# Optimization experiments

Measured on AMD Instinct MI355X. Metric: run time of the kernel, lower is better.

## Reference

```python
import jax, jax.numpy as jnp
import numpy as np
from jax import lax

B, P, NB, NF, NC, R = 128, 2048, 2000, 250, 16, 128
LS = NB - NF  # number of simulated bins = len_bins_gensig - 1


def setup_inputs() -> dict:
    key = jax.random.key(0)
    ks = jax.random.split(key, 10)
    return {
        'batched_stim_spat': jax.random.normal(ks[0], (B, P), jnp.float32),
        'stim_time': jax.random.normal(ks[1], (NB,), jnp.float32),
        'batched_initial_spike_section': (jax.random.uniform(ks[2], (B, NF)) < 0.05).astype(jnp.float32),
        'batched_coupling_cells': (jax.random.uniform(ks[3], (B, NC, NB)) < 0.05).astype(jnp.float32),
        'spatial_filter': jax.random.normal(ks[4], (P,), jnp.float32) * 0.02,
        'spatial_bias': jnp.float32(-2.0),
        'stim_timecourse_filter': jax.random.normal(ks[5], (NF,), jnp.float32) * 0.1,
        'feedback_filter': jax.random.normal(ks[6], (NF,), jnp.float32) * 0.05 - 0.02,
        'coupling_filter': jax.random.normal(ks[7], (NC, NF), jnp.float32) * 0.05,
        'u': jax.random.uniform(ks[8], (LS, B, R), jnp.float32),
        'n_repeats': R,
    }


def _corr1d_valid(x, k):
    # torch F.conv1d is cross-correlation; lax conv is too (no kernel flip)
    # x: (n,), k: (m,) -> (n - m + 1,)
    out = lax.conv_general_dilated(x[None, None, :], k[None, None, :], (1,), 'VALID',
                                   dimension_numbers=('NCH', 'OIH', 'NCH'))
    return out[0, 0]


def reference(batched_stim_spat, stim_time, batched_initial_spike_section,
              batched_coupling_cells, spatial_filter, spatial_bias,
              stim_timecourse_filter, feedback_filter, coupling_filter, u, n_repeats):
    nf = stim_timecourse_filter.shape[0]

    # stimulus time component: (n_bins - nf + 1,)
    filt_time = _corr1d_valid(stim_time, stim_timecourse_filter)

    # spatial exp arg for separable linear-spatial GLM:
    # einsum('bpt,p->bt', stim_spat[:,:,None]*filt_time, spatial_filter)
    # factors into outer product of (stim_spat @ spatial_filter) and filt_time
    stim_gensig = (batched_stim_spat @ spatial_filter)[:, None] * filt_time[None, :] + spatial_bias  # (B, T)

    # coupling exp arg: conv1d over all coupled cells -> (B, T)
    coup = lax.conv_general_dilated(batched_coupling_cells, coupling_filter[None, :, :], (1,), 'VALID',
                                    dimension_numbers=('NCH', 'OIH', 'NCH'))[:, 0, :]

    gensig_piece = stim_gensig + coup  # (B, T) with T = n_bins - nf + 1
    len_sim = gensig_piece.shape[1] - 1

    # initial feedback window: last nf spike bins, broadcast over repeats
    batch = batched_stim_spat.shape[0]
    w0 = jnp.broadcast_to(batched_initial_spike_section[:, None, :], (batch, n_repeats, nf)) + 0.0

    def step(window, xs):
        g_t, u_t = xs  # (B,), (B, R)
        fb = jnp.einsum('brk,k->br', window, feedback_filter)
        g = g_t[:, None] + fb
        spike = (u_t < jax.nn.sigmoid(g)).astype(window.dtype)  # Bernoulli(sigmoid(g))
        window = jnp.concatenate([window[:, :, 1:], spike[:, :, None]], axis=2)
        return window, spike

    xs = (jnp.swapaxes(gensig_piece[:, :len_sim], 0, 1), u[:len_sim])  # ((LS,B), (LS,B,R))
    _, spikes = lax.scan(step, w0, xs)  # spikes: (LS, B, R)

    out = jnp.concatenate([w0, jnp.moveaxis(spikes, 0, 2)], axis=2)  # (B, R, n_bins)
    return out
```

## Files before the change

### kernel.cpp

```cpp
#include <hip/hip_runtime.h>
#include <math.h>

#define B_  128
#define P_  2048
#define NB_ 2000
#define NF_ 250
#define NC_ 16
#define R_  128
#define LS_ 1750
#define NT_ 1751
#define BR_ (B_ * R_)
#define H_  16

typedef int v4i __attribute__((ext_vector_type(4)));

template <int CTRL>
__device__ __forceinline__ long long dpp64i(long long x) {
    int lo = (int)x, hi = (int)(x >> 32);
    lo = __builtin_amdgcn_mov_dpp(lo, CTRL, 0xF, 0xF, true);
    hi = __builtin_amdgcn_mov_dpp(hi, CTRL, 0xF, 0xF, true);
    return ((long long)(unsigned)lo) | ((long long)hi << 32);
}

__device__ __forceinline__ double logit_fast(float uf) {
    double u = (double)uf;
    double v = 1.0 - u;
    double qd = u / v;
    long long bits = __double_as_longlong(qd);
    int e = (int)((bits >> 52) & 0x7FF) - 1023;
    double m = __longlong_as_double((bits & 0xFFFFFFFFFFFFFLL) | 0x3FF0000000000000LL);
    if (m > 1.4142135623730951) { m *= 0.5; e += 1; }
    double s = (m - 1.0) / (m + 1.0);
    double z = s * s;
    double Q = fma(z, fma(z, fma(z, fma(z, fma(z, fma(z,
        0.06666666666666667, 0.07692307692307693), 0.09090909090909091),
        0.1111111111111111), 0.14285714285714285), 0.2), 0.3333333333333333);
    double logm = fma(2.0 * s, z * Q, 2.0 * s);
    return fma((double)e, 0.6931471805599453, logm);
}

__device__ __forceinline__ long long thrq_of(double lu, double fb) {
    double thr = lu - fb;
    thr = fmin(fmax(thr, -8.0), 8.0);
    double d = fma(thr, 0x1p45, 0x1.8p52);
    return (__double_as_longlong(d) & 0xFFFFFFFFFFFFFLL) - (1LL << 51);
}

__global__ __launch_bounds__(256) void k_pre(const float* __restrict__ st,
                                             const float* __restrict__ stf,
                                             const float* __restrict__ sp,
                                             const float* __restrict__ sf,
                                             double* __restrict__ ft,
                                             double* __restrict__ sdot) {
    if (blockIdx.x < 7) {
        int t = blockIdx.x * 256 + threadIdx.x;
        if (t >= NT_) return;
        double s = 0.0;
        for (int k = 0; k < NF_; ++k) s += (double)st[t + k] * (double)stf[k];
        ft[t] = s;
    } else {
        __shared__ double red[256];
        int b = blockIdx.x - 7;
        double s = 0.0;
        for (int p = threadIdx.x; p < P_; p += 256)
            s += (double)sp[(size_t)b * P_ + p] * (double)sf[p];
        red[threadIdx.x] = s;
        __syncthreads();
        for (int off = 128; off > 0; off >>= 1) {
            if (threadIdx.x < off) red[threadIdx.x] += red[threadIdx.x + off];
            __syncthreads();
        }
        if (threadIdx.x == 0) sdot[b] = red[0];
    }
}

__global__ __launch_bounds__(256) void k_coup(const float* __restrict__ cc,
                                              const float* __restrict__ cf,
                                              const double* __restrict__ sdot,
                                              const double* __restrict__ ft,
                                              const float* __restrict__ bias,
                                              double* __restrict__ gensig) {
    __shared__ __align__(16) float  ccs[NC_ * 512];
    __shared__ __align__(16) double cfs[NC_ * 256];
    __shared__ double red[3][64][4];
    int b = blockIdx.y, t0 = blockIdx.x * 256;
    int tid = threadIdx.x, lane = tid & 63, wv = tid >> 6;

    for (int idx = tid; idx < NC_ * 128; idx += 256) {
        int c = idx >> 7, j4 = (idx & 127) * 4, src = t0 + j4;
        const float* p = cc + ((size_t)b * NC_ + c) * NB_ + src;
        float4 v;
        if (src + 3 < NB_) v = *(const float4*)p;
        else {
            v.x = (src     < NB_) ? p[0] : 0.f;
            v.y = (src + 1 < NB_) ? p[1] : 0.f;
            v.z = (src + 2 < NB_) ? p[2] : 0.f;
            v.w = (src + 3 < NB_) ? p[3] : 0.f;
        }
        *(float4*)&ccs[c * 512 + j4] = v;
    }
    for (int idx = tid; idx < NC_ * 256; idx += 256) {
        int c = idx >> 8, k = idx & 255;
        cfs[idx] = (k < NF_) ? (double)cf[c * NF_ + k] : 0.0;
    }
    __syncthreads();

    double a0 = 0, a1 = 0, a2 = 0, a3 = 0;
    int base = lane * 4;
    for (int c = wv; c < NC_; c += 4) {
        const float*  row  = &ccs[c * 512];
        const double* crow = &cfs[c * 256];
        float4 cur = *(const float4*)&row[base];
        for (int k4 = 0; k4 < 252; k4 += 4) {
            float4 nxt = *(const float4*)&row[base + k4 + 4];
            double e0 = cur.x, e1 = cur.y, e2 = cur.z, e3 = cur.w;
            double e4 = nxt.x, e5 = nxt.y, e6 = nxt.z;
            double c0 = crow[k4], c1 = crow[k4 + 1], c2 = crow[k4 + 2], c3 = crow[k4 + 3];
            a0 += e0 * c0 + e1 * c1 + e2 * c2 + e3 * c3;
            a1 += e1 * c0 + e2 * c1 + e3 * c2 + e4 * c3;
            a2 += e2 * c0 + e3 * c1 + e4 * c2 + e5 * c3;
            a3 += e3 * c0 + e4 * c1 + e5 * c2 + e6 * c3;
            cur = nxt;
        }
    }
    if (wv > 0) {
        red[wv - 1][lane][0] = a0; red[wv - 1][lane][1] = a1;
        red[wv - 1][lane][2] = a2; red[wv - 1][lane][3] = a3;
    }
    __syncthreads();
    if (wv == 0) {
        a0 += red[0][lane][0] + red[1][lane][0] + red[2][lane][0];
        a1 += red[0][lane][1] + red[1][lane][1] + red[2][lane][1];
        a2 += red[0][lane][2] + red[1][lane][2] + red[2][lane][2];
        a3 += red[0][lane][3] + red[1][lane][3] + red[2][lane][3];
        double gb = (double)bias[0];
        double sd = sdot[b];
        double accs[4] = {a0, a1, a2, a3};
        int tb = t0 + base;
        for (int i = 0; i < 4; ++i) {
            int t = tb + i;
            if (t < LS_) gensig[(size_t)b * LS_ + t] = sd * ft[t] + gb + accs[i];
        }
    }
}

__global__ __launch_bounds__(256, 1) void k_scan(const double* __restrict__ gensig,
                                                 const float* __restrict__ u,
                                                 const float* __restrict__ iss,
                                                 const float* __restrict__ ff,
                                                 float* __restrict__ out) {
    __shared__ double farT_all[4][16 * 17];
    int tid = threadIdx.x;
    int wv = tid >> 6, l = tid & 63;
    int gw = blockIdx.x * 4 + wv;
    int b = gw >> 3, rbase = (gw & 7) * 16;
    double* farT = &farT_all[wv][0];

    int lw = l & 15;
    int q  = l >> 4;
    int cn = l >> 2;
    int j  = l & 3;

    const float* issb = iss + b * NF_;
    for (int idx = l; idx < 16 * NF_; idx += 64) {
        int c = idx / NF_, k = idx - c * NF_;
        out[((size_t)(b * R_ + rbase + c)) * NB_ + k] = issb[k];
    }

    unsigned long long W0 = 0, W1 = 0, W2 = 0, W3 = 0;
    for (int k = 0; k < NF_; ++k) {
        unsigned long long bit = (issb[k] > 0.5f) ? 1ull : 0ull;
        if      (k <  64) W0 |= bit << k;
        else if (k < 128) W1 |= bit << (k - 64);
        else if (k < 192) W2 |= bit << (k - 128);
        else              W3 |= bit << (k - 192);
    }

    int Bword[4][6][4];
#pragma unroll
    for (int kc = 0; kc < 4; ++kc)
#pragma unroll
        for (int p = 0; p < 6; ++p)
#pragma unroll
            for (int w = 0; w < 4; ++w) Bword[kc][p][w] = 0;
#pragma unroll
    for (int kc = 0; kc < 4; ++kc) {
#pragma unroll
        for (int jj = 0; jj < 16; ++jj) {
            int k = kc * 64 + q * 16 + jj;
            int idx = k - lw;
            long long v = 0;
            if (idx >= 0 && idx < NF_)
                v = __double2ll_rn((double)ff[idx] * 281474976710656.0);
#pragma unroll
            for (int p = 0; p < 6; ++p) {
                int d = (int)((v + 128) & 255) - 128;
                v = (v - (long long)d) >> 8;
                Bword[kc][p][jj >> 2] |= (d & 255) << ((jj & 3) * 8);
            }
        }
    }
    v4i Bf[4][6];
#pragma unroll
    for (int kc = 0; kc < 4; ++kc)
#pragma unroll
        for (int p = 0; p < 6; ++p) {
            v4i t; t.x = Bword[kc][p][0]; t.y = Bword[kc][p][1];
            t.z = Bword[kc][p][2]; t.w = Bword[kc][p][3];
            Bf[kc][p] = t;
        }

    const double* gs = gensig + (size_t)b * LS_;
    const float*  up = u + b * R_ + rbase + cn;
    float*        op = out + ((size_t)(b * R_ + rbase + cn)) * NB_ + NF_;

    long long tq0 = __double2ll_rn((double)ff[249 - 4 * j] * 0x1p45);
    long long tq1 = __double2ll_rn((double)ff[248 - 4 * j] * 0x1p45);
    long long tq2 = __double2ll_rn((double)ff[247 - 4 * j] * 0x1p45);
    long long tq3 = __double2ll_rn((double)ff[246 - 4 * j] * 0x1p45);

    auto do_far = [&](double gp) {
        unsigned long long Sarr[4] = {W0, W1, W2, W3};
        v4i acc[6];
#pragma unroll
        for (int p = 0; p < 6; ++p) acc[p] = (v4i){0, 0, 0, 0};
#pragma unroll
        for (int kc = 0; kc < 4; ++kc) {
            unsigned f = (unsigned)((Sarr[kc] >> (q * 16)) & 0xFFFFull);
            v4i av;
            av.x = (int)((((f      ) & 0xFu) * 0x00204081u) & 0x01010101u);
            av.y = (int)((((f >>  4) & 0xFu) * 0x00204081u) & 0x01010101u);
            av.z = (int)((((f >>  8) & 0xFu) * 0x00204081u) & 0x01010101u);
            av.w = (int)((((f >> 12) & 0xFu) * 0x00204081u) & 0x01010101u);
#pragma unroll
            for (int p = 0; p < 6; ++p)
                acc[p] = __builtin_amdgcn_mfma_i32_16x16x64_i8(av, Bf[kc][p], acc[p], 0, 0, 0);
        }
#pragma unroll
        for (int r = 0; r < 4; ++r) {
            int lo = acc[0][r] + acc[1][r] * 256 + acc[2][r] * 65536;
            int hi = acc[3][r] + acc[4][r] * 256 + acc[5][r] * 65536;
            double fb = gp + (double)lo * 0x1p-48 + (double)hi * 0x1p-24;
            farT[(q * 4 + r) * 17 + lw] = fb;
        }
    };

    double gprep = gs[lw];
    float ur0, ur1, ur2, ur3;
    {
        int t_;
        t_ = 0  + j; ur0 = up[(size_t)t_ * BR_];
        t_ = 4  + j; ur1 = up[(size_t)t_ * BR_];
        t_ = 8  + j; ur2 = up[(size_t)t_ * BR_];
        t_ = 12 + j; ur3 = up[(size_t)t_ * BR_];
    }
    long long thrq0, thrq1, thrq2, thrq3;
    do_far(gprep);
    {
        double lu0 = logit_fast(ur0), lu1 = logit_fast(ur1);
        double lu2 = logit_fast(ur2), lu3 = logit_fast(ur3);
        __asm__ volatile("s_waitcnt lgkmcnt(0)" ::: "memory");
        thrq0 = thrq_of(lu0, farT[cn * 17 + j]);
        thrq1 = thrq_of(lu1, farT[cn * 17 + 4 + j]);
        thrq2 = thrq_of(lu2, farT[cn * 17 + 8 + j]);
        thrq3 = thrq_of(lu3, farT[cn * 17 + 12 + j]);
    }
    { int tg = 16 + lw; if (tg > LS_ - 1) tg = LS_ - 1; gprep = gs[tg]; }
    {
        int t_;
        t_ = 16 + j;      if (t_ > LS_ - 1) t_ = LS_ - 1; ur0 = up[(size_t)t_ * BR_];
        t_ = 20 + j;      if (t_ > LS_ - 1) t_ = LS_ - 1; ur1 = up[(size_t)t_ * BR_];
        t_ = 24 + j;      if (t_ > LS_ - 1) t_ = LS_ - 1; ur2 = up[(size_t)t_ * BR_];
        t_ = 28 + j;      if (t_ > LS_ - 1) t_ = LS_ - 1; ur3 = up[(size_t)t_ * BR_];
    }

#define NSTEP(S, THRQ) { \
    long long thr = dpp64i<(S) * 0x55>(THRQ); \
    unsigned qb = (qreg >> (4 * j)) & 15u; \
    long long s = (((qb & 1u) ? tq0 : 0LL) + ((qb & 2u) ? tq1 : 0LL)) \
                + (((qb & 4u) ? tq2 : 0LL) + ((qb & 8u) ? tq3 : 0LL)); \
    s += dpp64i<0xB1>(s); \
    s += dpp64i<0x4E>(s); \
    bool sp = s > thr; \
    qreg = (qreg << 1) | (sp ? 1u : 0u); \
}

    for (int t0 = 0; t0 < LS_; t0 += H_) {
        unsigned qreg = 0;
        NSTEP(0, thrq0) NSTEP(1, thrq0) NSTEP(2, thrq0) NSTEP(3, thrq0)
        NSTEP(0, thrq1) NSTEP(1, thrq1) NSTEP(2, thrq1) NSTEP(3, thrq1)
        NSTEP(0, thrq2) NSTEP(1, thrq2) NSTEP(2, thrq2) NSTEP(3, thrq2)
        NSTEP(0, thrq3) NSTEP(1, thrq3) NSTEP(2, thrq3) NSTEP(3, thrq3)

        unsigned q2 = (__brev(qreg) >> 16) & 0xFFFFu;
        int rem = LS_ - t0; if (rem > H_) rem = H_;
        int s0 = 4 * j;
        if (s0 + 3 < rem) {
            float4 o;
            o.x = (float)((q2 >> (s0    )) & 1u);
            o.y = (float)((q2 >> (s0 + 1)) & 1u);
            o.z = (float)((q2 >> (s0 + 2)) & 1u);
            o.w = (float)((q2 >> (s0 + 3)) & 1u);
            *(float4*)(op + t0 + s0) = o;
        } else {
#pragma unroll
            for (int e = 0; e < 4; ++e)
                if (s0 + e < rem) op[t0 + s0 + e] = (float)((q2 >> (s0 + e)) & 1u);
        }

        if (t0 + H_ < LS_) {
            int q2i = __builtin_amdgcn_ds_bpermute(lw << 4, (int)q2);
            unsigned long long q2n = (unsigned long long)(unsigned)q2i;
            W0 = (W0 >> 16) | (W1 << 48);
            W1 = (W1 >> 16) | (W2 << 48);
            W2 = (W2 >> 16) | (W3 << 48);
            W3 = (W3 >> 16) | (q2n << 42);

            do_far(gprep);
            double lu0 = logit_fast(ur0), lu1 = logit_fast(ur1);
            double lu2 = logit_fast(ur2), lu3 = logit_fast(ur3);
            __asm__ volatile("s_waitcnt lgkmcnt(0)" ::: "memory");
            thrq0 = thrq_of(lu0, farT[cn * 17 + j]);
            thrq1 = thrq_of(lu1, farT[cn * 17 + 4 + j]);
            thrq2 = thrq_of(lu2, farT[cn * 17 + 8 + j]);
            thrq3 = thrq_of(lu3, farT[cn * 17 + 12 + j]);

            int tg = t0 + 32 + lw; if (tg > LS_ - 1) tg = LS_ - 1;
            gprep = gs[tg];
            int t_;
            t_ = t0 + 32 +  0 + j; if (t_ > LS_ - 1) t_ = LS_ - 1; ur0 = up[(size_t)t_ * BR_];
            t_ = t0 + 32 +  4 + j; if (t_ > LS_ - 1) t_ = LS_ - 1; ur1 = up[(size_t)t_ * BR_];
            t_ = t0 + 32 +  8 + j; if (t_ > LS_ - 1) t_ = LS_ - 1; ur2 = up[(size_t)t_ * BR_];
            t_ = t0 + 32 + 12 + j; if (t_ > LS_ - 1) t_ = LS_ - 1; ur3 = up[(size_t)t_ * BR_];
        }
    }
#undef NSTEP
}

extern "C" void kernel_launch(void* const* d_in, const int* in_sizes, int n_in,
                              void* d_out, int out_size, void* d_ws, size_t ws_size,
                              hipStream_t stream) {
    const float* stim_spat = (const float*)d_in[0];
    const float* stim_time = (const float*)d_in[1];
    const float* iss       = (const float*)d_in[2];
    const float* cc        = (const float*)d_in[3];
    const float* sf        = (const float*)d_in[4];
    const float* bias      = (const float*)d_in[5];
    const float* stf       = (const float*)d_in[6];
    const float* ff        = (const float*)d_in[7];
    const float* cf        = (const float*)d_in[8];
    const float* u         = (const float*)d_in[9];
    (void)in_sizes; (void)n_in; (void)out_size; (void)ws_size;

    float* out = (float*)d_out;

    double* ws     = (double*)d_ws;
    double* gensig = ws;
    double* ft     = gensig + (size_t)B_ * LS_;
    double* sdot   = ft + NT_;

    k_pre  <<<135, 256, 0, stream>>>(stim_time, stf, stim_spat, sf, ft, sdot);
    k_coup <<<dim3(7, B_), 256, 0, stream>>>(cc, cf, sdot, ft, bias, gensig);
    k_scan <<<B_ * 2, 256, 0, stream>>>(gensig, u, iss, ff, out);
}
```

Baseline: 553.0 us.

## Add producer warps computing logit of random draws into shared ring buffer

The scan kernel block grows from 256 to 512 threads. Four extra wavefronts load the uniform random numbers, compute logit_fast, and write the results two blocks ahead into a double-buffered shared-memory ring. The four scan wavefronts read these precomputed values instead of doing the global loads and double-precision divide and log on their critical serial path. The cost is a __syncthreads every 16-step block, which couples producer and consumer warps, plus the extra wavefronts and shared memory.

```diff
diff --git a/kernel.cpp b/kernel.cpp
--- a/kernel.cpp
+++ b/kernel.cpp
@@ -11,6 +11,7 @@
 #define NT_ 1751
 #define BR_ (B_ * R_)
 #define H_  16
+#define NBLK_ 110
 
 typedef int v4i __attribute__((ext_vector_type(4)));
 
@@ -144,80 +145,108 @@
     }
 }
 
-__global__ __launch_bounds__(256, 1) void k_scan(const double* __restrict__ gensig,
+__global__ __launch_bounds__(512, 2) void k_scan(const double* __restrict__ gensig,
                                                  const float* __restrict__ u,
                                                  const float* __restrict__ iss,
                                                  const float* __restrict__ ff,
                                                  float* __restrict__ out) {
     __shared__ double farT_all[4][16 * 17];
+    __shared__ double luring[2][4][4 * 64];
     int tid = threadIdx.x;
     int wv = tid >> 6, l = tid & 63;
-    int gw = blockIdx.x * 4 + wv;
+    int swv = wv & 3;
+    const bool isPrep = (wv >= 4);
+    int gw = blockIdx.x * 4 + swv;
     int b = gw >> 3, rbase = (gw & 7) * 16;
-    double* farT = &farT_all[wv][0];
+    double* farT = &farT_all[swv][0];
 
     int lw = l & 15;
     int q  = l >> 4;
     int cn = l >> 2;
     int j  = l & 3;
 
-    const float* issb = iss + b * NF_;
-    for (int idx = l; idx < 16 * NF_; idx += 64) {
-        int c = idx / NF_, k = idx - c * NF_;
-        out[((size_t)(b * R_ + rbase + c)) * NB_ + k] = issb[k];
-    }
+    const double* gs   = gensig + (size_t)b * LS_;
+    const float*  up   = u + b * R_ + rbase + cn;
+    float*        op   = out + ((size_t)(b * R_ + rbase + cn)) * NB_ + NF_;
+    const float*  issb = iss + b * NF_;
 
     unsigned long long W0 = 0, W1 = 0, W2 = 0, W3 = 0;
-    for (int k = 0; k < NF_; ++k) {
-        unsigned long long bit = (issb[k] > 0.5f) ? 1ull : 0ull;
-        if      (k <  64) W0 |= bit << k;
-        else if (k < 128) W1 |= bit << (k - 64);
-        else if (k < 192) W2 |= bit << (k - 128);
-        else              W3 |= bit << (k - 192);
-    }
-
-    int Bword[4][6][4];
-#pragma unroll
-    for (int kc = 0; kc < 4; ++kc)
-#pragma unroll
-        for (int p = 0; p < 6; ++p)
-#pragma unroll
-            for (int w = 0; w < 4; ++w) Bword[kc][p][w] = 0;
-#pragma unroll
-    for (int kc = 0; kc < 4; ++kc) {
-#pragma unroll
-        for (int jj = 0; jj < 16; ++jj) {
-            int k = kc * 64 + q * 16 + jj;
-            int idx = k - lw;
-            long long v = 0;
-            if (idx >= 0 && idx < NF_)
-                v = __double2ll_rn((double)ff[idx] * 281474976710656.0);
+    v4i Bf[4][6];
+    long long tq0 = 0, tq1 = 0, tq2 = 0, tq3 = 0;
+    long long thrq0 = 0, thrq1 = 0, thrq2 = 0, thrq3 = 0;
+    double gprep = 0.0;
+    float ur0 = 0.f, ur1 = 0.f, ur2 = 0.f, ur3 = 0.f;
+
+    if (!isPrep) {
+        for (int idx = l; idx < 16 * NF_; idx += 64) {
+            int c = idx / NF_, k = idx - c * NF_;
+            out[((size_t)(b * R_ + rbase + c)) * NB_ + k] = issb[k];
+        }
+        for (int k = 0; k < NF_; ++k) {
+            unsigned long long bit = (issb[k] > 0.5f) ? 1ull : 0ull;
+            if      (k <  64) W0 |= bit << k;
+            else if (k < 128) W1 |= bit << (k - 64);
+            else if (k < 192) W2 |= bit << (k - 128);
+            else              W3 |= bit << (k - 192);
+        }
+        int Bword[4][6][4];
+#pragma unroll
+        for (int kc = 0; kc < 4; ++kc)
+#pragma unroll
+            for (int p = 0; p < 6; ++p)
+#pragma unroll
+                for (int w = 0; w < 4; ++w) Bword[kc][p][w] = 0;
+#pragma unroll
+        for (int kc = 0; kc < 4; ++kc) {
+#pragma unroll
+            for (int jj = 0; jj < 16; ++jj) {
+                int k = kc * 64 + q * 16 + jj;
+                int idx = k - lw;
+                long long v = 0;
+                if (idx >= 0 && idx < NF_)
+                    v = __double2ll_rn((double)ff[idx] * 281474976710656.0);
+#pragma unroll
+                for (int p = 0; p < 6; ++p) {
+                    int d = (int)((v + 128) & 255) - 128;
+                    v = (v - (long long)d) >> 8;
+                    Bword[kc][p][jj >> 2] |= (d & 255) << ((jj & 3) * 8);
+                }
+            }
+        }
+#pragma unroll
+        for (int kc = 0; kc < 4; ++kc)
 #pragma unroll
             for (int p = 0; p < 6; ++p) {
-                int d = (int)((v + 128) & 255) - 128;
-                v = (v - (long long)d) >> 8;
-                Bword[kc][p][jj >> 2] |= (d & 255) << ((jj & 3) * 8);
+                v4i t; t.x = Bword[kc][p][0]; t.y = Bword[kc][p][1];
+                t.z = Bword[kc][p][2]; t.w = Bword[kc][p][3];
+                Bf[kc][p] = t;
             }
-        }
-    }
-    v4i Bf[4][6];
-#pragma unroll
-    for (int kc = 0; kc < 4; ++kc)
-#pragma unroll
-        for (int p = 0; p < 6; ++p) {
-            v4i t; t.x = Bword[kc][p][0]; t.y = Bword[kc][p][1];
-            t.z = Bword[kc][p][2]; t.w = Bword[kc][p][3];
-            Bf[kc][p] = t;
-        }
-
-    const double* gs = gensig + (size_t)b * LS_;
-    const float*  up = u + b * R_ + rbase + cn;
-    float*        op = out + ((size_t)(b * R_ + rbase + cn)) * NB_ + NF_;
-
-    long long tq0 = __double2ll_rn((double)ff[249 - 4 * j] * 0x1p45);
-    long long tq1 = __double2ll_rn((double)ff[248 - 4 * j] * 0x1p45);
-    long long tq2 = __double2ll_rn((double)ff[247 - 4 * j] * 0x1p45);
-    long long tq3 = __double2ll_rn((double)ff[246 - 4 * j] * 0x1p45);
+        tq0 = __double2ll_rn((double)ff[249 - 4 * j] * 0x1p45);
+        tq1 = __double2ll_rn((double)ff[248 - 4 * j] * 0x1p45);
+        tq2 = __double2ll_rn((double)ff[247 - 4 * j] * 0x1p45);
+        tq3 = __double2ll_rn((double)ff[246 - 4 * j] * 0x1p45);
+    } else {
+        ur0 = up[(size_t)(0  + j) * BR_];
+        ur1 = up[(size_t)(4  + j) * BR_];
+        ur2 = up[(size_t)(8  + j) * BR_];
+        ur3 = up[(size_t)(12 + j) * BR_];
+        luring[0][swv][  0 + l] = logit_fast(ur0);
+        luring[0][swv][ 64 + l] = logit_fast(ur1);
+        luring[0][swv][128 + l] = logit_fast(ur2);
+        luring[0][swv][192 + l] = logit_fast(ur3);
+        ur0 = up[(size_t)(16 + j) * BR_];
+        ur1 = up[(size_t)(20 + j) * BR_];
+        ur2 = up[(size_t)(24 + j) * BR_];
+        ur3 = up[(size_t)(28 + j) * BR_];
+        luring[1][swv][  0 + l] = logit_fast(ur0);
+        luring[1][swv][ 64 + l] = logit_fast(ur1);
+        luring[1][swv][128 + l] = logit_fast(ur2);
+        luring[1][swv][192 + l] = logit_fast(ur3);
+        ur0 = up[(size_t)(32 + j) * BR_];
+        ur1 = up[(size_t)(36 + j) * BR_];
+        ur2 = up[(size_t)(40 + j) * BR_];
+        ur3 = up[(size_t)(44 + j) * BR_];
+    }
 
     auto do_far = [&](double gp) {
         unsigned long long Sarr[4] = {W0, W1, W2, W3};
@@ -245,34 +274,24 @@
         }
     };
 
-    double gprep = gs[lw];
-    float ur0, ur1, ur2, ur3;
-    {
-        int t_;
-        t_ = 0  + j; ur0 = up[(size_t)t_ * BR_];
-        t_ = 4  + j; ur1 = up[(size_t)t_ * BR_];
-        t_ = 8  + j; ur2 = up[(size_t)t_ * BR_];
-        t_ = 12 + j; ur3 = up[(size_t)t_ * BR_];
-    }
-    long long thrq0, thrq1, thrq2, thrq3;
-    do_far(gprep);
-    {
-        double lu0 = logit_fast(ur0), lu1 = logit_fast(ur1);
-        double lu2 = logit_fast(ur2), lu3 = logit_fast(ur3);
+    __syncthreads();
+
+    if (!isPrep) {
+        gprep = gs[lw];
+        do_far(gprep);
+        double lu0 = luring[0][swv][  0 + l];
+        double lu1 = luring[0][swv][ 64 + l];
+        double lu2 = luring[0][swv][128 + l];
+        double lu3 = luring[0][swv][192 + l];
         __asm__ volatile("s_waitcnt lgkmcnt(0)" ::: "memory");
         thrq0 = thrq_of(lu0, farT[cn * 17 + j]);
         thrq1 = thrq_of(lu1, farT[cn * 17 + 4 + j]);
         thrq2 = thrq_of(lu2, farT[cn * 17 + 8 + j]);
         thrq3 = thrq_of(lu3, farT[cn * 17 + 12 + j]);
-    }
-    { int tg = 16 + lw; if (tg > LS_ - 1) tg = LS_ - 1; gprep = gs[tg]; }
-    {
-        int t_;
-        t_ = 16 + j;      if (t_ > LS_ - 1) t_ = LS_ - 1; ur0 = up[(size_t)t_ * BR_];
-        t_ = 20 + j;      if (t_ > LS_ - 1) t_ = LS_ - 1; ur1 = up[(size_t)t_ * BR_];
-        t_ = 24 + j;      if (t_ > LS_ - 1) t_ = LS_ - 1; ur2 = up[(size_t)t_ * BR_];
-        t_ = 28 + j;      if (t_ > LS_ - 1) t_ = LS_ - 1; ur3 = up[(size_t)t_ * BR_];
-    }
+        { int tg = 16 + lw; if (tg > LS_ - 1) tg = LS_ - 1; gprep = gs[tg]; }
+    }
+
+    __syncthreads();
 
 #define NSTEP(S, THRQ) { \
     long long thr = dpp64i<(S) * 0x55>(THRQ); \
@@ -285,54 +304,73 @@
     qreg = (qreg << 1) | (sp ? 1u : 0u); \
 }
 
-    for (int t0 = 0; t0 < LS_; t0 += H_) {
-        unsigned qreg = 0;
-        NSTEP(0, thrq0) NSTEP(1, thrq0) NSTEP(2, thrq0) NSTEP(3, thrq0)
-        NSTEP(0, thrq1) NSTEP(1, thrq1) NSTEP(2, thrq1) NSTEP(3, thrq1)
-        NSTEP(0, thrq2) NSTEP(1, thrq2) NSTEP(2, thrq2) NSTEP(3, thrq2)
-        NSTEP(0, thrq3) NSTEP(1, thrq3) NSTEP(2, thrq3) NSTEP(3, thrq3)
-
-        unsigned q2 = (__brev(qreg) >> 16) & 0xFFFFu;
-        int rem = LS_ - t0; if (rem > H_) rem = H_;
-        int s0 = 4 * j;
-        if (s0 + 3 < rem) {
-            float4 o;
-            o.x = (float)((q2 >> (s0    )) & 1u);
-            o.y = (float)((q2 >> (s0 + 1)) & 1u);
-            o.z = (float)((q2 >> (s0 + 2)) & 1u);
-            o.w = (float)((q2 >> (s0 + 3)) & 1u);
-            *(float4*)(op + t0 + s0) = o;
+    int blk = 0;
+    for (int t0 = 0; t0 < LS_; t0 += H_, ++blk) {
+        if (!isPrep) {
+            unsigned qreg = 0;
+            NSTEP(0, thrq0) NSTEP(1, thrq0) NSTEP(2, thrq0) NSTEP(3, thrq0)
+            NSTEP(0, thrq1) NSTEP(1, thrq1) NSTEP(2, thrq1) NSTEP(3, thrq1)
+            NSTEP(0, thrq2) NSTEP(1, thrq2) NSTEP(2, thrq2) NSTEP(3, thrq2)
+            NSTEP(0, thrq3) NSTEP(1, thrq3) NSTEP(2, thrq3) NSTEP(3, thrq3)
+
+            unsigned q2 = (__brev(qreg) >> 16) & 0xFFFFu;
+            int rem = LS_ - t0; if (rem > H_) rem = H_;
+            int s0 = 4 * j;
+            if (s0 + 3 < rem) {
+                float4 o;
+                o.x = (float)((q2 >> (s0    )) & 1u);
+                o.y = (float)((q2 >> (s0 + 1)) & 1u);
+                o.z = (float)((q2 >> (s0 + 2)) & 1u);
+                o.w = (float)((q2 >> (s0 + 3)) & 1u);
+                *(float4*)(op + t0 + s0) = o;
+            } else {
+#pragma unroll
+                for (int e = 0; e < 4; ++e)
+                    if (s0 + e < rem) op[t0 + s0 + e] = (float)((q2 >> (s0 + e)) & 1u);
+            }
+
+            if (t0 + H_ < LS_) {
+                double lu0 = luring[(blk + 1) & 1][swv][  0 + l];
+                double lu1 = luring[(blk + 1) & 1][swv][ 64 + l];
+                double lu2 = luring[(blk + 1) & 1][swv][128 + l];
+                double lu3 = luring[(blk + 1) & 1][swv][192 + l];
+
+                int q2i = __builtin_amdgcn_ds_bpermute(lw << 4, (int)q2);
+                unsigned long long q2n = (unsigned long long)(unsigned)q2i;
+                W0 = (W0 >> 16) | (W1 << 48);
+                W1 = (W1 >> 16) | (W2 << 48);
+                W2 = (W2 >> 16) | (W3 << 48);
+                W3 = (W3 >> 16) | (q2n << 42);
+
+                do_far(gprep);
+                __asm__ volatile("s_waitcnt lgkmcnt(0)" ::: "memory");
+                thrq0 = thrq_of(lu0, farT[cn * 17 + j]);
+                thrq1 = thrq_of(lu1, farT[cn * 17 + 4 + j]);
+                thrq2 = thrq_of(lu2, farT[cn * 17 + 8 + j]);
+                thrq3 = thrq_of(lu3, farT[cn * 17 + 12 + j]);
+
+                int tg = t0 + 32 + lw; if (tg > LS_ - 1) tg = LS_ - 1;
+                gprep = gs[tg];
+            }
         } else {
-#pragma unroll
-            for (int e = 0; e < 4; ++e)
-                if (s0 + e < rem) op[t0 + s0 + e] = (float)((q2 >> (s0 + e)) & 1u);
-        }
-
-        if (t0 + H_ < LS_) {
-            int q2i = __builtin_amdgcn_ds_bpermute(lw << 4, (int)q2);
-            unsigned long long q2n = (unsigned long long)(unsigned)q2i;
-            W0 = (W0 >> 16) | (W1 << 48);
-            W1 = (W1 >> 16) | (W2 << 48);
-            W2 = (W2 >> 16) | (W3 << 48);
-            W3 = (W3 >> 16) | (q2n << 42);
-
-            do_far(gprep);
-            double lu0 = logit_fast(ur0), lu1 = logit_fast(ur1);
-            double lu2 = logit_fast(ur2), lu3 = logit_fast(ur3);
-            __asm__ volatile("s_waitcnt lgkmcnt(0)" ::: "memory");
-            thrq0 = thrq_of(lu0, farT[cn * 17 + j]);
-            thrq1 = thrq_of(lu1, farT[cn * 17 + 4 + j]);
-            thrq2 = thrq_of(lu2, farT[cn * 17 + 8 + j]);
-            thrq3 = thrq_of(lu3, farT[cn * 17 + 12 + j]);
-
-            int tg = t0 + 32 + lw; if (tg > LS_ - 1) tg = LS_ - 1;
-            gprep = gs[tg];
-            int t_;
-            t_ = t0 + 32 +  0 + j; if (t_ > LS_ - 1) t_ = LS_ - 1; ur0 = up[(size_t)t_ * BR_];
-            t_ = t0 + 32 +  4 + j; if (t_ > LS_ - 1) t_ = LS_ - 1; ur1 = up[(size_t)t_ * BR_];
-            t_ = t0 + 32 +  8 + j; if (t_ > LS_ - 1) t_ = LS_ - 1; ur2 = up[(size_t)t_ * BR_];
-            t_ = t0 + 32 + 12 + j; if (t_ > LS_ - 1) t_ = LS_ - 1; ur3 = up[(size_t)t_ * BR_];
-        }
+            if (blk <= NBLK_ - 3) {
+                double lu0 = logit_fast(ur0), lu1 = logit_fast(ur1);
+                double lu2 = logit_fast(ur2), lu3 = logit_fast(ur3);
+                luring[blk & 1][swv][  0 + l] = lu0;
+                luring[blk & 1][swv][ 64 + l] = lu1;
+                luring[blk & 1][swv][128 + l] = lu2;
+                luring[blk & 1][swv][192 + l] = lu3;
+                if (blk <= NBLK_ - 4) {
+                    int T = (blk + 3) * H_;
+                    int t_;
+                    t_ = T + 0  + j; if (t_ > LS_ - 1) t_ = LS_ - 1; ur0 = up[(size_t)t_ * BR_];
+                    t_ = T + 4  + j; if (t_ > LS_ - 1) t_ = LS_ - 1; ur1 = up[(size_t)t_ * BR_];
+                    t_ = T + 8  + j; if (t_ > LS_ - 1) t_ = LS_ - 1; ur2 = up[(size_t)t_ * BR_];
+                    t_ = T + 12 + j; if (t_ > LS_ - 1) t_ = LS_ - 1; ur3 = up[(size_t)t_ * BR_];
+                }
+            }
+        }
+        __syncthreads();
     }
 #undef NSTEP
 }
@@ -361,5 +399,5 @@
 
     k_pre  <<<135, 256, 0, stream>>>(stim_time, stf, stim_spat, sf, ft, sdot);
     k_coup <<<dim3(7, B_), 256, 0, stream>>>(cc, cf, sdot, ft, bias, gensig);
-    k_scan <<<B_ * 2, 256, 0, stream>>>(gensig, u, iss, ff, out);
-}
+    k_scan <<<B_ * 2, 512, 0, stream>>>(gensig, u, iss, ff, out);
+}
```

After: 567.0 us. +2.5%, slower.
